# Kernel tuning notes

Hardware: AMD Instinct MI355X
Metric: run time of the kernel (lower is better)

The kernel has to match this reference:

```python
import jax, jax.numpy as jnp
import numpy as np

B, T, D = 2, 2048, 1024
H = 16
HD = D // H  # head dim == config.k == config.v == 64


def setup_inputs() -> dict:
    key = jax.random.key(0)
    k1, k2, k3 = jax.random.split(key, 3)
    scale = 0.02
    x = jax.random.normal(k1, (B, T, D), dtype=jnp.float32)
    W1 = jax.random.normal(k2, (D, 3 * D), dtype=jnp.float32) * scale
    b1 = jnp.zeros((3 * D,), dtype=jnp.float32)
    W2 = jax.random.normal(k3, (D, D), dtype=jnp.float32) * scale
    b2 = jnp.zeros((D,), dtype=jnp.float32)
    return {"x": x, "W1": W1, "b1": b1, "W2": W2, "b2": b2}


def reference(x, W1, b1, W2, b2):
    # Fused QKV projection (dropout layers are identity in eval mode).
    Bx, Tx, C = x.shape
    qkv = x @ W1 + b1                      # [B, T, 3D]
    q, k, v = jnp.split(qkv, 3, axis=-1)   # each [B, T, D]
    q = q.reshape(Bx, Tx, H, HD).transpose(0, 2, 1, 3)  # [B, H, T, hd]
    k = k.reshape(Bx, Tx, H, HD).transpose(0, 2, 1, 3)
    v = v.reshape(Bx, Tx, H, HD).transpose(0, 2, 1, 3)

    logits = jnp.einsum('bhmk,bhnk->bhmn', q, k) / jnp.sqrt(jnp.float32(HD))
    # causal mask (lower-triangular bias buffer)
    causal = jnp.tril(jnp.ones((Tx, Tx), dtype=bool))
    logits = jnp.where(causal[None, None], logits, jnp.float32(-jnp.inf))
    att = jax.nn.softmax(logits, axis=-1)   # [B, H, T, T]

    y = jnp.einsum('bhmn,bhnv->bhmv', att, v)        # [B, H, T, hd]
    y = y.transpose(0, 2, 1, 3).reshape(Bx, Tx, C)   # [B, T, D]
    return y @ W2 + b2
```

## Files before the change

### kernel.cpp

```cpp
#include <hip/hip_runtime.h>

typedef __attribute__((ext_vector_type(8))) short bf16x8;
typedef __attribute__((ext_vector_type(4))) float f32x4;
typedef __attribute__((ext_vector_type(16))) float f32x16;
typedef __attribute__((ext_vector_type(4))) short short4v;
typedef __attribute__((ext_vector_type(4))) unsigned int uint4v;

#define B_  2
#define T_  2048
#define D_  1024
#define H_  16
#define HD_ 64

__device__ inline short f2bf(float f){
  unsigned u = __builtin_bit_cast(unsigned, f);
  u += 0x7fff + ((u >> 16) & 1);
  return (short)(u >> 16);
}
__device__ inline float bf2f(short s){
  unsigned u = ((unsigned)(unsigned short)s) << 16;
  return __builtin_bit_cast(float, u);
}

__device__ inline void gl2lds16(const void* g, void* l){
  __builtin_amdgcn_global_load_lds(
      (const __attribute__((address_space(1))) unsigned int*)g,
      (__attribute__((address_space(3))) unsigned int*)l, 16, 0, 0);
}

__device__ inline void transpose_tile(const float* __restrict__ in,
                                      short* __restrict__ out,
                                      int R, int C, int bx, int by){
  __shared__ float tile[32][33];
  int tx = threadIdx.x & 31, ty0 = threadIdx.x >> 5;
#pragma unroll
  for (int i = 0; i < 4; i++){
    int ty = ty0 + i * 8;
    tile[ty][tx] = in[(by + ty) * C + bx + tx];
  }
  __syncthreads();
#pragma unroll
  for (int i = 0; i < 4; i++){
    int ty = ty0 + i * 8;
    out[(bx + ty) * R + by + tx] = f2bf(tile[tx][ty]);
  }
}

__global__ __launch_bounds__(256) void prep(
    const float* __restrict__ x,  short* __restrict__ xb,
    const float* __restrict__ W1, short* __restrict__ W1T,
    const float* __restrict__ W2, short* __restrict__ W2T){
  const int bid = blockIdx.x;
  if (bid < 4096){
    int i = (bid * 256 + threadIdx.x) * 4;
    float4 v = *(const float4*)(x + i);
    short4v o;
    o[0] = f2bf(v.x); o[1] = f2bf(v.y); o[2] = f2bf(v.z); o[3] = f2bf(v.w);
    *(short4v*)(xb + i) = o;
  } else if (bid < 4096 + 3072){
    int tb = bid - 4096;
    transpose_tile(W1, W1T, 1024, 3072, (tb % 96) << 5, (tb / 96) << 5);
  } else {
    int tb = bid - 7168;
    transpose_tile(W2, W2T, 1024, 1024, (tb % 32) << 5, (tb / 32) << 5);
  }
}

#define BM 128
#define BN 128
#define BK 32

#define QSCALE 0.18033688011112042f

template<int N_, int K_, int EPI>
__global__ __launch_bounds__(256, 3) void gemm_bt(
    const short* __restrict__ A, const short* __restrict__ Bt,
    const float* __restrict__ bias,
    short* __restrict__ q, short* __restrict__ kk, short* __restrict__ vT,
    float* __restrict__ outf){
  __shared__ short As[3][BM * BK];
  __shared__ short Bs[3][BN * BK];
  const int tid = threadIdx.x;
  const int lane = tid & 63, w = tid >> 6;
  const int wm = w >> 1, wn = w & 1;
  const int lr = lane & 15, lk = lane >> 4;
  const int brow = blockIdx.y * BM, bcol = blockIdx.x * BN;
  f32x4 acc[4][4] = {};
  const short* Ag = A  + brow * K_;
  const short* Bg = Bt + bcol * K_;

  auto stage = [&](int buf, int k0){
#pragma unroll
    for (int i = 0; i < 2; i++){
      int idx = i * 256 + tid;
      int row = idx >> 2, c8 = (idx & 3) * 8;
      gl2lds16(Ag + row * K_ + k0 + c8, (char*)As[buf] + idx * 16);
      gl2lds16(Bg + row * K_ + k0 + c8, (char*)Bs[buf] + idx * 16);
    }
  };

  const int NT = K_ / BK;
  stage(0, 0);
  stage(1, BK);
  for (int t = 0; t < NT; ++t){
    if (t + 1 < NT)
      asm volatile("s_waitcnt vmcnt(4)" ::: "memory");
    else
      asm volatile("s_waitcnt vmcnt(0)" ::: "memory");
    __builtin_amdgcn_s_barrier();
    __builtin_amdgcn_sched_barrier(0);
    if (t + 2 < NT)
      stage((t + 2) % 3, (t + 2) * BK);
    __builtin_amdgcn_sched_barrier(0);

    const short* Ac = As[t % 3];
    const short* Bc = Bs[t % 3];
    bf16x8 a[4], b[4];
#pragma unroll
    for (int mf = 0; mf < 4; mf++)
      a[mf] = *(const bf16x8*)(Ac + (wm * 64 + mf * 16 + lr) * BK + lk * 8);
#pragma unroll
    for (int nf = 0; nf < 4; nf++)
      b[nf] = *(const bf16x8*)(Bc + (wn * 64 + nf * 16 + lr) * BK + lk * 8);
    __builtin_amdgcn_s_setprio(1);
#pragma unroll
    for (int mf = 0; mf < 4; mf++)
#pragma unroll
      for (int nf = 0; nf < 4; nf++)
        acc[mf][nf] = __builtin_amdgcn_mfma_f32_16x16x32_bf16(a[mf], b[nf], acc[mf][nf], 0, 0, 0);
    __builtin_amdgcn_s_setprio(0);
  }

  if constexpr (EPI == 0){
#pragma unroll
    for (int nf = 0; nf < 4; nf++){
      int n = bcol + wn * 64 + nf * 16 + lr;
      float bv = bias[n];
      int sec = n >> 10, d = n & 1023, h = d >> 6, hd = d & 63;
#pragma unroll
      for (int mf = 0; mf < 4; mf++){
        int m0 = brow + wm * 64 + mf * 16 + lk * 4;
        int b = m0 >> 11, t0 = m0 & 2047;
        int bh = b * H_ + h;
        if (sec == 0){
#pragma unroll
          for (int r = 0; r < 4; r++)
            q[(bh * T_ + t0 + r) * HD_ + hd] = f2bf((acc[mf][nf][r] + bv) * QSCALE);
        } else if (sec == 1){
#pragma unroll
          for (int r = 0; r < 4; r++)
            kk[(bh * T_ + t0 + r) * HD_ + hd] = f2bf(acc[mf][nf][r] + bv);
        } else {
          float v0 = acc[mf][nf][0] + bv, v1 = acc[mf][nf][1] + bv;
          float v2 = acc[mf][nf][2] + bv, v3 = acc[mf][nf][3] + bv;
          unsigned lo = (unsigned)(unsigned short)f2bf(v0) | ((unsigned)(unsigned short)f2bf(v1) << 16);
          unsigned hi = (unsigned)(unsigned short)f2bf(v2) | ((unsigned)(unsigned short)f2bf(v3) << 16);
          uint2 pk; pk.x = lo; pk.y = hi;
          *(uint2*)(vT + (bh * HD_ + hd) * T_ + t0) = pk;
        }
      }
    }
  } else {
#pragma unroll
    for (int nf = 0; nf < 4; nf++){
      int n = bcol + wn * 64 + nf * 16 + lr;
      float bv = bias[n];
#pragma unroll
      for (int mf = 0; mf < 4; mf++){
        int m0 = brow + wm * 64 + mf * 16 + lk * 4;
#pragma unroll
        for (int r = 0; r < 4; r++)
          outf[(m0 + r) * N_ + n] = acc[mf][nf][r] + bv;
      }
    }
  }
}

__device__ inline int crow(int r, int h){ return (r & 3) + 8 * (r >> 2) + 4 * h; }

template<int NS>
__global__ __launch_bounds__(256, 4) void attn32(
    const short* __restrict__ Q, const short* __restrict__ Kg,
    const short* __restrict__ Vt, short* __restrict__ Y,
    short* __restrict__ Op, float* __restrict__ ml){
  __shared__ short Ks[2][64 * 64];
  __shared__ short Vs[2][64 * 64];
  __shared__ float bounce[4][32];
  const int tid = threadIdx.x;
  const int w = tid >> 6, l = tid & 63;
  const int lq = l & 31, h = l >> 5;
  const int bx = blockIdx.x;
  int i, hf;
  if constexpr (NS == 4){
    int u = bx >> 5, v = u & 15;
    i = (v < 8) ? 15 - v : v - 8;
    hf = u >> 4;
  } else {
    i = (bx < 256) ? 15 - (bx >> 5) : (bx >> 5) - 8;
    hf = 0;
  }
  const int bh = bx & 31;
  const int q0 = i * 128, qw = q0 + w * 32;
  const int nt = 2 * (i + 1);
  const int t0 = hf * nt / NS;
  const int t1 = (hf + 1) * nt / NS;

  bf16x8 qb[4];
  {
    const short* qbase = Q + (bh * T_ + qw + lq) * HD_;
#pragma unroll
    for (int dk = 0; dk < 4; dk++)
      qb[dk] = *(const bf16x8*)(qbase + dk * 16 + h * 8);
  }

  f32x16 o0 = {}, o1 = {};
  float m = -1e30f, ll = 0.f;

  auto stage = [&](int buf, int t){
#pragma unroll
    for (int j = 0; j < 2; j++){
      int idx = j * 256 + tid;
      int row = idx >> 3, cb = (idx & 7) * 16;
      int cbs = cb ^ ((row & 7) << 4);
      gl2lds16(Kg + (bh * T_ + t * 64 + row) * HD_ + (cbs >> 1), (char*)Ks[buf] + idx * 16);
      gl2lds16(Vt + (bh * HD_ + row) * T_ + t * 64 + (cbs >> 1), (char*)Vs[buf] + idx * 16);
    }
  };

  if (t0 < t1){
    stage(0, t0);
    for (int t = t0; t < t1; ++t){
      const int cur = (t - t0) & 1;
      if (t + 1 < t1){
        stage(cur ^ 1, t + 1);
        asm volatile("s_waitcnt vmcnt(4)" ::: "memory");
      } else {
        asm volatile("s_waitcnt vmcnt(0)" ::: "memory");
      }
      __builtin_amdgcn_s_barrier();
      __builtin_amdgcn_sched_barrier(0);

      const int kvb = t * 64;
      if (kvb <= qw + 31){
        const short* Kc = Ks[cur];
        const short* Vc = Vs[cur];

        f32x16 s[2] = {};
        __builtin_amdgcn_s_setprio(1);
#pragma unroll
        for (int kb = 0; kb < 2; kb++){
          int row = kb * 32 + lq;
          const char* rp = (const char*)Kc + row * 128;
          int swz = (row & 7) << 4;
#pragma unroll
          for (int dk = 0; dk < 4; dk++){
            bf16x8 ka = *(const bf16x8*)(rp + ((dk * 32 + h * 16) ^ swz));
            s[kb] = __builtin_amdgcn_mfma_f32_32x32x16_bf16(ka, qb[dk], s[kb], 0, 0, 0);
          }
        }
        __builtin_amdgcn_s_setprio(0);

        const int qg = qw + lq;
        if (kvb + 63 > qw){
#pragma unroll
          for (int kb = 0; kb < 2; kb++)
#pragma unroll
            for (int r = 0; r < 16; r++){
              int kv = kvb + kb * 32 + crow(r, h);
              if (kv > qg) s[kb][r] = -1e30f;
            }
        }

        float pm = s[0][0];
#pragma unroll
        for (int r = 1; r < 16; r++) pm = fmaxf(pm, s[0][r]);
#pragma unroll
        for (int r = 0; r < 16; r++) pm = fmaxf(pm, s[1][r]);
        pm = fmaxf(pm, __shfl_xor(pm, 32));

        if (__any(pm > m + 8.f)){
          float mn = fmaxf(pm, m);
          float sf = __builtin_amdgcn_exp2f(m - mn);
          m = mn;
          ll *= sf;
          bounce[w][lq] = sf;
#pragma unroll
          for (int r = 0; r < 16; r++){
            float sr = bounce[w][crow(r, h)];
            o0[r] *= sr; o1[r] *= sr;
          }
        }

        float ts = 0.f;
#pragma unroll
        for (int kb = 0; kb < 2; kb++)
#pragma unroll
          for (int r = 0; r < 16; r++){
            float p = __builtin_amdgcn_exp2f(s[kb][r] - m);
            s[kb][r] = p;
            ts += p;
          }
        ts += __shfl_xor(ts, 32);
        ll += ts;

        unsigned pw0[8], pw1[8];
#pragma unroll
        for (int kb = 0; kb < 2; kb++)
#pragma unroll
          for (int gg = 0; gg < 4; gg++){
            unsigned r0, r1;
            asm("v_cvt_pk_bf16_f32 %0, %1, %2" : "=v"(r0) : "v"(s[kb][gg * 4 + 0]), "v"(s[kb][gg * 4 + 1]));
            asm("v_cvt_pk_bf16_f32 %0, %1, %2" : "=v"(r1) : "v"(s[kb][gg * 4 + 2]), "v"(s[kb][gg * 4 + 3]));
            pw0[kb * 4 + gg] = r0;
            pw1[kb * 4 + gg] = r1;
          }
#pragma unroll
        for (int ks = 0; ks < 4; ks++){
          asm("v_permlane32_swap_b32 %0, %1" : "+v"(pw0[2 * ks]), "+v"(pw0[2 * ks + 1]));
          asm("v_permlane32_swap_b32 %0, %1" : "+v"(pw1[2 * ks]), "+v"(pw1[2 * ks + 1]));
        }

        __builtin_amdgcn_s_setprio(1);
#pragma unroll
        for (int ks = 0; ks < 4; ks++){
          uint4v paw;
          paw[0] = pw0[2 * ks];     paw[1] = pw1[2 * ks];
          paw[2] = pw0[2 * ks + 1]; paw[3] = pw1[2 * ks + 1];
          bf16x8 pa = __builtin_bit_cast(bf16x8, paw);
#pragma unroll
          for (int nb = 0; nb < 2; nb++){
            int row = nb * 32 + lq;
            bf16x8 vb = *(const bf16x8*)((const char*)Vc + row * 128 +
                          ((ks * 32 + h * 16) ^ ((row & 7) << 4)));
            if (nb == 0) o0 = __builtin_amdgcn_mfma_f32_32x32x16_bf16(pa, vb, o0, 0, 0, 0);
            else         o1 = __builtin_amdgcn_mfma_f32_32x32x16_bf16(pa, vb, o1, 0, 0, 0);
          }
        }
        __builtin_amdgcn_s_setprio(0);
      }
      __builtin_amdgcn_sched_barrier(0);
      __builtin_amdgcn_s_barrier();
    }
  }

  if constexpr (NS == 4){
    short* Oq = Op + ((size_t)(hf * 32 + bh)) * (size_t)T_ * 64;
    if (h == 0){
      float* mlr = ml + ((size_t)(hf * 32 + bh) * T_ + (qw + lq)) * 2;
      mlr[0] = m; mlr[1] = ll;
    }
#pragma unroll
    for (int r = 0; r < 16; r++){
      int qg = qw + crow(r, h);
      Oq[qg * 64 + lq]      = f2bf(o0[r]);
      Oq[qg * 64 + 32 + lq] = f2bf(o1[r]);
    }
  } else {
    bounce[w][lq] = __builtin_amdgcn_rcpf(ll);
    const int b = bh >> 4, hh = bh & 15;
#pragma unroll
    for (int r = 0; r < 16; r++){
      int row = crow(r, h);
      float rl = bounce[w][row];
      int qg = qw + row;
      short* yb = Y + (b * T_ + qg) * D_ + hh * 64;
      yb[lq]      = f2bf(o0[r] * rl);
      yb[32 + lq] = f2bf(o1[r] * rl);
    }
  }
}

__global__ __launch_bounds__(256) void attn_merge(
    const short* __restrict__ Op, const float* __restrict__ ml,
    short* __restrict__ Y){
  int gid = blockIdx.x * 256 + threadIdx.x;
  int rid = gid >> 2, c16 = (gid & 3) * 16;
  float mh[4], lh[4];
#pragma unroll
  for (int hf = 0; hf < 4; hf++){
    float2 v = *(const float2*)(ml + (size_t)hf * 131072 + rid * 2);
    mh[hf] = v.x; lh[hf] = v.y;
  }
  float M = fmaxf(fmaxf(mh[0], mh[1]), fmaxf(mh[2], mh[3]));
  float f[4], den = 0.f;
#pragma unroll
  for (int hf = 0; hf < 4; hf++){
    f[hf] = __builtin_amdgcn_exp2f(mh[hf] - M);
    den += f[hf] * lh[hf];
  }
  float rl = 1.f / den;
  float acc[16] = {};
#pragma unroll
  for (int hf = 0; hf < 4; hf++){
    const short* o = Op + (size_t)hf * 4194304 + (size_t)rid * 64 + c16;
    bf16x8 a = *(const bf16x8*)(o);
    bf16x8 b = *(const bf16x8*)(o + 8);
    float fh = f[hf];
#pragma unroll
    for (int j = 0; j < 8; j++){
      acc[j]     += fh * bf2f(a[j]);
      acc[8 + j] += fh * bf2f(b[j]);
    }
  }
  int bh = rid >> 11, t = rid & 2047;
  short* yb = Y + (((bh >> 4) * T_ + t) * D_) + (bh & 15) * 64 + c16;
  bf16x8 o0, o1;
#pragma unroll
  for (int j = 0; j < 8; j++){
    o0[j] = f2bf(acc[j] * rl);
    o1[j] = f2bf(acc[8 + j] * rl);
  }
  *(bf16x8*)(yb)     = o0;
  *(bf16x8*)(yb + 8) = o1;
}

extern "C" void kernel_launch(void* const* d_in, const int* in_sizes, int n_in,
                              void* d_out, int out_size, void* d_ws, size_t ws_size,
                              hipStream_t stream) {
  const float* x  = (const float*)d_in[0];
  const float* W1 = (const float*)d_in[1];
  const float* b1 = (const float*)d_in[2];
  const float* W2 = (const float*)d_in[3];
  const float* b2 = (const float*)d_in[4];
  float* out = (float*)d_out;

  char* ws = (char*)d_ws;
  short* W1T = (short*)(ws);
  short* W2T = (short*)(ws + 6291456);
  short* xb  = (short*)(ws + 8388608);
  short* q   = (short*)(ws + 16777216);
  short* kk  = (short*)(ws + 25165824);
  short* vT  = (short*)(ws + 33554432);
  short* Op  = (short*)(ws + 41943040);
  float* mlb = (float*)(ws);
  short* y   = xb;

  const size_t need = 41943040ull + 33554432ull;
  const bool split = ws_size >= need;

  prep<<<dim3(8192), dim3(256), 0, stream>>>(x, xb, W1, W1T, W2, W2T);
  gemm_bt<3072, 1024, 0><<<dim3(24, 32), dim3(256), 0, stream>>>(xb, W1T, b1, q, kk, vT, nullptr);
  if (split){
    attn32<4><<<dim3(2048), dim3(256), 0, stream>>>(q, kk, vT, nullptr, Op, mlb);
    attn_merge<<<dim3(1024), dim3(256), 0, stream>>>(Op, mlb, y);
  } else {
    attn32<1><<<dim3(512), dim3(256), 0, stream>>>(q, kk, vT, y, nullptr, nullptr);
  }
  gemm_bt<1024, 1024, 1><<<dim3(8, 32), dim3(256), 0, stream>>>(y, W2T, b2, nullptr, nullptr, nullptr, out);
}
```

Measured before the change: 111.5 us.

## Replace QKV GEMM with 256x192 tile, 8-wave kernel and swizzled LDS

Adds a dedicated QKV projection kernel that uses 512 threads, 256x192 output tiles and BK=64 double-buffered LDS with an XOR swizzle to avoid bank conflicts. Global-to-LDS prefetch is interleaved across four MFMA phases, with explicit barriers between them. The grid becomes 16x16=256 blocks, roughly one per CU, which raises operand reuse per block. In exchange, occupancy drops and wave quantization on 256 CUs becomes a risk. The generic GEMM is reduced to the output-projection epilogue only.

```diff
diff --git a/kernel.cpp b/kernel.cpp
--- a/kernel.cpp
+++ b/kernel.cpp
@@ -66,18 +66,140 @@
   }
 }
 
+#define QSCALE 0.18033688011112042f
+
+__global__ __launch_bounds__(512) void gemm_qkv8(
+    const short* __restrict__ A, const short* __restrict__ Bt,
+    const float* __restrict__ bias,
+    short* __restrict__ q, short* __restrict__ kk, short* __restrict__ vT){
+  constexpr int K_ = 1024, NT = K_ / 64;
+  __shared__ short As[2][256 * 64];
+  __shared__ short Bs[2][192 * 64];
+  const int tid = threadIdx.x;
+  const int lane = tid & 63, w = tid >> 6;
+  const int wm = w >> 2, wn = w & 3;
+  const int lr = lane & 15, lk = lane >> 4;
+  const int brow = blockIdx.y * 256, bcol = blockIdx.x * 192;
+  const short* Ag = A  + brow * K_;
+  const short* Bg = Bt + bcol * K_;
+  f32x4 acc[8][3] = {};
+
+  auto stageA = [&](int buf, int k0, int j){
+    int idx = j * 512 + tid;
+    int row = idx >> 3, cb = (idx & 7) * 16;
+    int cs = cb ^ ((row & 7) << 4);
+    gl2lds16(Ag + row * K_ + k0 + (cs >> 1), (char*)As[buf] + idx * 16);
+  };
+  auto stageB = [&](int buf, int k0, int j){
+    int idx = j * 512 + tid;
+    int row = idx >> 3, cb = (idx & 7) * 16;
+    int cs = cb ^ ((row & 7) << 4);
+    gl2lds16(Bg + row * K_ + k0 + (cs >> 1), (char*)Bs[buf] + idx * 16);
+  };
+
+#pragma unroll
+  for (int j = 0; j < 4; j++) stageA(0, 0, j);
+#pragma unroll
+  for (int j = 0; j < 3; j++) stageB(0, 0, j);
+  asm volatile("s_waitcnt vmcnt(0)" ::: "memory");
+  __builtin_amdgcn_s_barrier();
+  __builtin_amdgcn_sched_barrier(0);
+
+  for (int t = 0; t < NT; ++t){
+    const int cur = t & 1;
+    const short* Ac = As[cur];
+    const short* Bc = Bs[cur];
+    const int nk0 = (t + 1) * 64;
+    const bool pf = (t + 1 < NT);
+    bf16x8 b[3][2];
+#pragma unroll
+    for (int p = 0; p < 4; p++){
+      if (p == 0){
+#pragma unroll
+        for (int nf = 0; nf < 3; nf++){
+          int rrow = wn * 48 + nf * 16 + lr;
+          const char* rp = (const char*)Bc + rrow * 128;
+          int swz = (rrow & 7) << 4;
+#pragma unroll
+          for (int kx = 0; kx < 2; kx++)
+            b[nf][kx] = *(const bf16x8*)(rp + ((kx * 64 + lk * 16) ^ swz));
+        }
+      }
+      bf16x8 a[2][2];
+#pragma unroll
+      for (int mf = 0; mf < 2; mf++){
+        int arow = wm * 128 + p * 32 + mf * 16 + lr;
+        const char* rp = (const char*)Ac + arow * 128;
+        int swz = (arow & 7) << 4;
+#pragma unroll
+        for (int kx = 0; kx < 2; kx++)
+          a[mf][kx] = *(const bf16x8*)(rp + ((kx * 64 + lk * 16) ^ swz));
+      }
+      if (pf){
+        if (p == 0){ stageA(cur ^ 1, nk0, 0); stageA(cur ^ 1, nk0, 1); }
+        else if (p == 1){ stageA(cur ^ 1, nk0, 2); stageA(cur ^ 1, nk0, 3); }
+        else if (p == 2){ stageB(cur ^ 1, nk0, 0); stageB(cur ^ 1, nk0, 1); }
+        else          {  stageB(cur ^ 1, nk0, 2); }
+      }
+      __builtin_amdgcn_sched_barrier(0);
+      __builtin_amdgcn_s_barrier();
+      __builtin_amdgcn_sched_barrier(0);
+      __builtin_amdgcn_s_setprio(1);
+#pragma unroll
+      for (int mf = 0; mf < 2; mf++)
+#pragma unroll
+        for (int nf = 0; nf < 3; nf++)
+#pragma unroll
+          for (int kx = 0; kx < 2; kx++)
+            acc[p * 2 + mf][nf] = __builtin_amdgcn_mfma_f32_16x16x32_bf16(
+                a[mf][kx], b[nf][kx], acc[p * 2 + mf][nf], 0, 0, 0);
+      __builtin_amdgcn_s_setprio(0);
+      __builtin_amdgcn_sched_barrier(0);
+      if (p == 3 && pf)
+        asm volatile("s_waitcnt vmcnt(0)" ::: "memory");
+      __builtin_amdgcn_s_barrier();
+      __builtin_amdgcn_sched_barrier(0);
+    }
+  }
+
+#pragma unroll
+  for (int nf = 0; nf < 3; nf++){
+    int n = bcol + wn * 48 + nf * 16 + lr;
+    float bv = bias[n];
+    int sec = n >> 10, d = n & 1023, h = d >> 6, hd = d & 63;
+#pragma unroll
+    for (int qd = 0; qd < 8; qd++){
+      int m0 = brow + wm * 128 + qd * 16 + lk * 4;
+      int bb = m0 >> 11, t0 = m0 & 2047;
+      int bh = bb * H_ + h;
+      if (sec == 0){
+#pragma unroll
+        for (int r = 0; r < 4; r++)
+          q[(bh * T_ + t0 + r) * HD_ + hd] = f2bf((acc[qd][nf][r] + bv) * QSCALE);
+      } else if (sec == 1){
+#pragma unroll
+        for (int r = 0; r < 4; r++)
+          kk[(bh * T_ + t0 + r) * HD_ + hd] = f2bf(acc[qd][nf][r] + bv);
+      } else {
+        float v0 = acc[qd][nf][0] + bv, v1 = acc[qd][nf][1] + bv;
+        float v2 = acc[qd][nf][2] + bv, v3 = acc[qd][nf][3] + bv;
+        unsigned lo = (unsigned)(unsigned short)f2bf(v0) | ((unsigned)(unsigned short)f2bf(v1) << 16);
+        unsigned hi = (unsigned)(unsigned short)f2bf(v2) | ((unsigned)(unsigned short)f2bf(v3) << 16);
+        uint2 pk; pk.x = lo; pk.y = hi;
+        *(uint2*)(vT + (bh * HD_ + hd) * T_ + t0) = pk;
+      }
+    }
+  }
+}
+
 #define BM 128
 #define BN 128
 #define BK 32
 
-#define QSCALE 0.18033688011112042f
-
-template<int N_, int K_, int EPI>
+template<int N_, int K_>
 __global__ __launch_bounds__(256, 3) void gemm_bt(
     const short* __restrict__ A, const short* __restrict__ Bt,
-    const float* __restrict__ bias,
-    short* __restrict__ q, short* __restrict__ kk, short* __restrict__ vT,
-    float* __restrict__ outf){
+    const float* __restrict__ bias, float* __restrict__ outf){
   __shared__ short As[3][BM * BK];
   __shared__ short Bs[3][BN * BK];
   const int tid = threadIdx.x;
@@ -131,47 +253,16 @@
     __builtin_amdgcn_s_setprio(0);
   }
 
-  if constexpr (EPI == 0){
-#pragma unroll
-    for (int nf = 0; nf < 4; nf++){
-      int n = bcol + wn * 64 + nf * 16 + lr;
-      float bv = bias[n];
-      int sec = n >> 10, d = n & 1023, h = d >> 6, hd = d & 63;
-#pragma unroll
-      for (int mf = 0; mf < 4; mf++){
-        int m0 = brow + wm * 64 + mf * 16 + lk * 4;
-        int b = m0 >> 11, t0 = m0 & 2047;
-        int bh = b * H_ + h;
-        if (sec == 0){
-#pragma unroll
-          for (int r = 0; r < 4; r++)
-            q[(bh * T_ + t0 + r) * HD_ + hd] = f2bf((acc[mf][nf][r] + bv) * QSCALE);
-        } else if (sec == 1){
-#pragma unroll
-          for (int r = 0; r < 4; r++)
-            kk[(bh * T_ + t0 + r) * HD_ + hd] = f2bf(acc[mf][nf][r] + bv);
-        } else {
-          float v0 = acc[mf][nf][0] + bv, v1 = acc[mf][nf][1] + bv;
-          float v2 = acc[mf][nf][2] + bv, v3 = acc[mf][nf][3] + bv;
-          unsigned lo = (unsigned)(unsigned short)f2bf(v0) | ((unsigned)(unsigned short)f2bf(v1) << 16);
-          unsigned hi = (unsigned)(unsigned short)f2bf(v2) | ((unsigned)(unsigned short)f2bf(v3) << 16);
-          uint2 pk; pk.x = lo; pk.y = hi;
-          *(uint2*)(vT + (bh * HD_ + hd) * T_ + t0) = pk;
-        }
-      }
-    }
-  } else {
-#pragma unroll
-    for (int nf = 0; nf < 4; nf++){
-      int n = bcol + wn * 64 + nf * 16 + lr;
-      float bv = bias[n];
-#pragma unroll
-      for (int mf = 0; mf < 4; mf++){
-        int m0 = brow + wm * 64 + mf * 16 + lk * 4;
-#pragma unroll
-        for (int r = 0; r < 4; r++)
-          outf[(m0 + r) * N_ + n] = acc[mf][nf][r] + bv;
-      }
+#pragma unroll
+  for (int nf = 0; nf < 4; nf++){
+    int n = bcol + wn * 64 + nf * 16 + lr;
+    float bv = bias[n];
+#pragma unroll
+    for (int mf = 0; mf < 4; mf++){
+      int m0 = brow + wm * 64 + mf * 16 + lk * 4;
+#pragma unroll
+      for (int r = 0; r < 4; r++)
+        outf[(m0 + r) * N_ + n] = acc[mf][nf][r] + bv;
     }
   }
 }
@@ -439,12 +530,12 @@
   const bool split = ws_size >= need;
 
   prep<<<dim3(8192), dim3(256), 0, stream>>>(x, xb, W1, W1T, W2, W2T);
-  gemm_bt<3072, 1024, 0><<<dim3(24, 32), dim3(256), 0, stream>>>(xb, W1T, b1, q, kk, vT, nullptr);
+  gemm_qkv8<<<dim3(16, 16), dim3(512), 0, stream>>>(xb, W1T, b1, q, kk, vT);
   if (split){
     attn32<4><<<dim3(2048), dim3(256), 0, stream>>>(q, kk, vT, nullptr, Op, mlb);
     attn_merge<<<dim3(1024), dim3(256), 0, stream>>>(Op, mlb, y);
   } else {
     attn32<1><<<dim3(512), dim3(256), 0, stream>>>(q, kk, vT, y, nullptr, nullptr);
   }
-  gemm_bt<1024, 1024, 1><<<dim3(8, 32), dim3(256), 0, stream>>>(y, W2T, b2, nullptr, nullptr, nullptr, out);
-}
+  gemm_bt<1024, 1024><<<dim3(8, 32), dim3(256), 0, stream>>>(y, W2T, b2, out);
+}
```

New measurement: 112.2 us. No clear change (+0.6%).
